# Kernel tuning notes

Measured on AMD Instinct MI355X. Metric: run time of the kernel, lower is better.

## Reference

```python
import jax, jax.numpy as jnp
import numpy as np

P = 1.0  # Yager t-norm exponent (tnorm_p)


def _patches(x, k):
    # x: [B, C, H, W] -> [B, C*k*k, Ho, Wo], feature ordering (c, kh, kw) like torch unfold
    B, C, H, W = x.shape
    Ho, Wo = H - k + 1, W - k + 1
    cols = [x[:, :, i:i + Ho, j:j + Wo] for i in range(k) for j in range(k)]
    p = jnp.stack(cols, axis=2)  # [B, C, k*k, Ho, Wo]
    return p.reshape(B, C * k * k, Ho, Wo)


def _max_yager2d(x, w, p):
    # Fuzzy conv: Yager t-norm T(a,b)=max(0, 1-((1-a)^p+(1-b)^p)^(1/p)) between each
    # patch element and kernel weight, aggregated with max over the receptive field.
    O, C, k, _ = w.shape
    pat = _patches(x, k)                       # [B, L, Ho, Wo], L = C*k*k
    wf = w.reshape(O, -1)                      # [O, L]
    a = 1.0 - pat[:, None]                     # [B, 1, L, Ho, Wo]
    b = 1.0 - wf[None, :, :, None, None]       # [1, O, L, 1, 1]
    t = jnp.maximum(0.0, 1.0 - (a ** p + b ** p) ** (1.0 / p))
    return jnp.max(t, axis=2)                  # [B, O, Ho, Wo]


def _maxpool2(x):
    return jax.lax.reduce_window(x, -jnp.inf, jax.lax.max,
                                 (1, 1, 2, 2), (1, 1, 2, 2), 'VALID')


def setup_inputs() -> dict:
    key = jax.random.key(0)
    k1, k2, k3, k4, k5, k6, k7 = jax.random.split(key, 7)
    B = 128
    inputs = jax.random.uniform(k1, (B, 3, 32, 32), dtype=jnp.float32)
    # fuzzy kernels are membership values in [0,1]
    w1 = jax.random.uniform(k2, (6, 3, 5, 5), dtype=jnp.float32)
    w2 = jax.random.uniform(k3, (16, 6, 5, 5), dtype=jnp.float32)
    w3 = jax.random.uniform(k4, (120, 16, 5, 5), dtype=jnp.float32)
    wd = jax.random.normal(k5, (120, 84), dtype=jnp.float32) * 0.1  # DenseDefuzzy weights
    wf = jax.random.normal(k6, (84, 10), dtype=jnp.float32) * 0.1   # fc5 weight
    bf = jax.random.normal(k7, (10,), dtype=jnp.float32) * 0.01     # fc5 bias
    return {"inputs": inputs, "w1": w1, "w2": w2, "w3": w3,
            "wd": wd, "wf": wf, "bf": bf}


def reference(inputs, w1, w2, w3, wd, wf, bf):
    x = _maxpool2(_max_yager2d(inputs, w1, P))   # [B,6,14,14]
    x = _maxpool2(_max_yager2d(x, w2, P))        # [B,16,5,5]
    x = _max_yager2d(x, w3, P)                   # [B,120,1,1]
    x = x.reshape(x.shape[0], -1)                # [B,120]
    x = jnp.tanh(x @ wd)                         # DenseDefuzzy (unnormalized) + tanh
    return jax.nn.log_softmax(x @ wf + bf, axis=-1)
```

## Files before the change

### kernel.cpp

```cpp
#include <hip/hip_runtime.h>
#include <math.h>


#define NT 1024
#define ROWS 34
#define PLANE (32 * ROWS)

__global__ __launch_bounds__(NT) void fused_lenet(
    const float* __restrict__ x,
    const float* __restrict__ w1,
    const float* __restrict__ w2,
    const float* __restrict__ w3,
    const float* __restrict__ wd,
    const float* __restrict__ wf,
    const float* __restrict__ bfv,
    float* __restrict__ out)
{
    const int img = blockIdx.x;
    const int tid = threadIdx.x;

    __shared__ float s_in[3 * PLANE];
    __shared__ float s_w1d[648];
    __shared__ float s_w2d[3456];
    __shared__ unsigned s_a1u[1176];
    __shared__ unsigned s_a2u[400];
    __shared__ float s_a3[120];
    __shared__ float s_a4[84];

    {
        const float2* src = (const float2*)(x + img * 3072);
        for (int i = tid; i < 1536; i += NT) {
            const int c = i >> 9, rem = i & 511, r = rem >> 4, col2 = rem & 15;
            ((float2*)s_in)[c * (PLANE / 2) + r * (ROWS / 2) + col2] = src[i];
        }
        for (int i = tid; i < 1176; i += NT) s_a1u[i] = 0u;
        if (tid < 400) s_a2u[tid] = 0u;

        for (int e = tid; e < 4104; e += NT) {
            const float* raw;
            float* dst;
            int v;
            if (e < 648) {
                const int oc = e / 108, u = e - oc * 108;
                const int c = u / 36; v = u - c * 36;
                raw = w1 + (oc * 3 + c) * 25;
                dst = s_w1d + e;
            } else {
                const int idx = e - 648;
                const int oc = idx / 216, u = idx - oc * 216;
                const int c = u / 36; v = u - c * 36;
                raw = w2 + (oc * 6 + c) * 25;
                dst = s_w2d + idx;
            }
            const int r = v / 6, col = v - r * 6;
            float m = -1e30f;
            #pragma unroll
            for (int dy = 0; dy < 2; ++dy) {
                const int kh = r - dy;
                if ((unsigned)kh > 4u) continue;
                #pragma unroll
                for (int dx = 0; dx < 2; ++dx) {
                    const int kw = col - dx;
                    if ((unsigned)kw > 4u) continue;
                    m = fmaxf(m, raw[kh * 5 + kw]);
                }
            }
            *dst = m;
        }
    }
    __syncthreads();

    if (tid < 1008) {
        const int c = tid / 336;
        const int rr = tid - c * 336;
        const int oc = rr / 56;
        const int r2 = rr - oc * 56;
        const int py = r2 >> 2;
        const int s = (r2 >> 1) & 1;
        const int h = r2 & 1;
        float acc[7];
        #pragma unroll
        for (int j = 0; j < 7; ++j) acc[j] = -1e30f;
        const float* wbase = s_w1d + (oc * 3 + c) * 36 + h * 18;
        const float* xbase = s_in + c * PLANE + (2 * py + 3 * h) * ROWS + 14 * s;
        #pragma unroll
        for (int u = 0; u < 3; ++u) {
            const float* xr = xbase + u * ROWS;
            float xv[18];
            #pragma unroll
            for (int i2 = 0; i2 < 9; ++i2)
                ((float2*)xv)[i2] = ((const float2*)xr)[i2];
            float wv[6];
            #pragma unroll
            for (int i2 = 0; i2 < 3; ++i2)
                ((float2*)wv)[i2] = ((const float2*)(wbase + u * 6))[i2];
            #pragma unroll
            for (int j = 0; j < 7; ++j) {
                #pragma unroll
                for (int ux = 0; ux < 6; ++ux)
                    acc[j] = fmaxf(acc[j], xv[2 * j + ux] + wv[ux]);
            }
        }
        const int obase = oc * 196 + py * 14 + 7 * s;
        #pragma unroll
        for (int j = 0; j < 7; ++j) {
            const float rl = fmaxf(acc[j] - 1.0f, 0.0f);
            atomicMax(&s_a1u[obase + j], __float_as_uint(rl));
        }
    }
    __syncthreads();

    if (tid < 960) {
        const int oc = tid / 60;
        const int rr = tid - oc * 60;
        const int py = rr / 12;
        const int r2 = rr - py * 12;
        const int c = r2 >> 1;
        const int h = r2 & 1;
        float acc[5];
        #pragma unroll
        for (int j = 0; j < 5; ++j) acc[j] = -1e30f;
        const float* a1f = (const float*)s_a1u;
        const float* wbase = s_w2d + (oc * 6 + c) * 36 + h * 18;
        const float* xbase = a1f + c * 196 + (2 * py + 3 * h) * 14;
        #pragma unroll
        for (int u = 0; u < 3; ++u) {
            const float* xr = xbase + u * 14;
            float xv[14];
            #pragma unroll
            for (int i2 = 0; i2 < 7; ++i2)
                ((float2*)xv)[i2] = ((const float2*)xr)[i2];
            float wv[6];
            #pragma unroll
            for (int i2 = 0; i2 < 3; ++i2)
                ((float2*)wv)[i2] = ((const float2*)(wbase + u * 6))[i2];
            #pragma unroll
            for (int j = 0; j < 5; ++j) {
                #pragma unroll
                for (int ux = 0; ux < 6; ++ux)
                    acc[j] = fmaxf(acc[j], xv[2 * j + ux] + wv[ux]);
            }
        }
        const int obase = oc * 25 + py * 5;
        #pragma unroll
        for (int j = 0; j < 5; ++j) {
            const float rl = fmaxf(acc[j] - 1.0f, 0.0f);
            atomicMax(&s_a2u[obase + j], __float_as_uint(rl));
        }
    }
    __syncthreads();

    if (tid < 960) {
        const int o = tid >> 3, q = tid & 7;
        const float4* wv = (const float4*)(w3 + o * 400);
        const float4* av = (const float4*)(const float*)s_a2u;
        float m = -1e30f;
        for (int l = q; l < 100; l += 8) {
            const float4 w = wv[l];
            const float4 a = av[l];
            m = fmaxf(m, fmaxf(fmaxf(a.x + w.x, a.y + w.y),
                               fmaxf(a.z + w.z, a.w + w.w)));
        }
        m = fmaxf(m, __shfl_xor(m, 1));
        m = fmaxf(m, __shfl_xor(m, 2));
        m = fmaxf(m, __shfl_xor(m, 4));
        if (q == 0) s_a3[o] = fmaxf(m - 1.0f, 0.0f);
    }
    __syncthreads();

    if (tid < 672) {
        const int o = tid >> 3, q = tid & 7;
        float acc = 0.0f;
        #pragma unroll 5
        for (int i = 0; i < 15; ++i) {
            const int k = q * 15 + i;
            acc = fmaf(s_a3[k], wd[k * 84 + o], acc);
        }
        acc += __shfl_xor(acc, 1);
        acc += __shfl_xor(acc, 2);
        acc += __shfl_xor(acc, 4);
        if (q == 0) s_a4[o] = tanhf(acc);
    }
    __syncthreads();

    if (tid < 64) {
        float acc = 0.0f;
        if (tid < 40) {
            const int o = tid >> 2, q = tid & 3;
            #pragma unroll 7
            for (int i = 0; i < 21; ++i) {
                const int k = q * 21 + i;
                acc = fmaf(s_a4[k], wf[k * 10 + o], acc);
            }
            acc += __shfl_xor(acc, 1);
            acc += __shfl_xor(acc, 2);
            acc += bfv[o];
        }
        const float lg = __shfl(acc, (tid < 10) ? tid * 4 : 0);
        if (tid < 16) {
            float v = (tid < 10) ? lg : -1e30f;
            #pragma unroll
            for (int d = 1; d < 16; d <<= 1)
                v = fmaxf(v, __shfl_xor(v, d));
            float e = (tid < 10) ? expf(lg - v) : 0.0f;
            float ssum = e;
            #pragma unroll
            for (int d = 1; d < 16; d <<= 1)
                ssum += __shfl_xor(ssum, d);
            if (tid < 10)
                out[img * 10 + tid] = lg - v - logf(ssum);
        }
    }
}

extern "C" void kernel_launch(void* const* d_in, const int* in_sizes, int n_in,
                              void* d_out, int out_size, void* d_ws, size_t ws_size,
                              hipStream_t stream) {
    const float* x   = (const float*)d_in[0];
    const float* w1  = (const float*)d_in[1];
    const float* w2  = (const float*)d_in[2];
    const float* w3  = (const float*)d_in[3];
    const float* wd  = (const float*)d_in[4];
    const float* wf  = (const float*)d_in[5];
    const float* bfv = (const float*)d_in[6];
    float* out = (float*)d_out;

    const int B = in_sizes[0] / (3 * 32 * 32);
    fused_lenet<<<dim3(B), dim3(NT), 0, stream>>>(
        x, w1, w2, w3, wd, wf, bfv, out);
}
```

Before: 81.91 us.

## Prefetch w3 and wd into registers early and defer w2 preprocessing

Loads the layer-3 weights (13 float4 per thread) into registers at kernel start and the dense weights before the layer-3 barrier, so their global-memory latency overlaps the conv stages instead of stalling the later small stages. Moves the dilated/pooled w2 table build after conv1, so it runs alongside conv1 atomics before the barrier. For the layer-3 loop, out-of-range indices are clamped to the last element, which leaves the max unchanged. The cost is more register pressure (52+15 extra VGPRs) in a 1024-thread block, which risks spills or lower occupancy.

Measured after the change: 78.10 us. 4.6% less time.

```diff
diff --git a/kernel.cpp b/kernel.cpp
--- a/kernel.cpp
+++ b/kernel.cpp
@@ -27,6 +27,17 @@
     __shared__ float s_a3[120];
     __shared__ float s_a4[84];
 
+    float4 w3p[13];
+    if (tid < 960) {
+        const int o = tid >> 3, q = tid & 7;
+        const float4* wv = (const float4*)(w3 + o * 400);
+        #pragma unroll
+        for (int i = 0; i < 13; ++i) {
+            int l = q + 8 * i; if (l > 99) l = 99;
+            w3p[i] = wv[l];
+        }
+    }
+
     {
         const float2* src = (const float2*)(x + img * 3072);
         for (int i = tid; i < 1536; i += NT) {
@@ -35,24 +46,11 @@
         }
         for (int i = tid; i < 1176; i += NT) s_a1u[i] = 0u;
         if (tid < 400) s_a2u[tid] = 0u;
-
-        for (int e = tid; e < 4104; e += NT) {
-            const float* raw;
-            float* dst;
-            int v;
-            if (e < 648) {
-                const int oc = e / 108, u = e - oc * 108;
-                const int c = u / 36; v = u - c * 36;
-                raw = w1 + (oc * 3 + c) * 25;
-                dst = s_w1d + e;
-            } else {
-                const int idx = e - 648;
-                const int oc = idx / 216, u = idx - oc * 216;
-                const int c = u / 36; v = u - c * 36;
-                raw = w2 + (oc * 6 + c) * 25;
-                dst = s_w2d + idx;
-            }
+        if (tid < 648) {
+            const int oc = tid / 108, u = tid - oc * 108;
+            const int c = u / 36, v = u - c * 36;
             const int r = v / 6, col = v - r * 6;
+            const float* raw = w1 + (oc * 3 + c) * 25;
             float m = -1e30f;
             #pragma unroll
             for (int dy = 0; dy < 2; ++dy) {
@@ -65,7 +63,7 @@
                     m = fmaxf(m, raw[kh * 5 + kw]);
                 }
             }
-            *dst = m;
+            s_w1d[tid] = m;
         }
     }
     __syncthreads();
@@ -108,6 +106,25 @@
             atomicMax(&s_a1u[obase + j], __float_as_uint(rl));
         }
     }
+    for (int e = tid; e < 3456; e += NT) {
+        const int oc = e / 216, u = e - oc * 216;
+        const int c = u / 36, v = u - c * 36;
+        const int r = v / 6, col = v - r * 6;
+        const float* raw = w2 + (oc * 6 + c) * 25;
+        float m = -1e30f;
+        #pragma unroll
+        for (int dy = 0; dy < 2; ++dy) {
+            const int kh = r - dy;
+            if ((unsigned)kh > 4u) continue;
+            #pragma unroll
+            for (int dx = 0; dx < 2; ++dx) {
+                const int kw = col - dx;
+                if ((unsigned)kw > 4u) continue;
+                m = fmaxf(m, raw[kh * 5 + kw]);
+            }
+        }
+        s_w2d[e] = m;
+    }
     __syncthreads();
 
     if (tid < 960) {
@@ -148,16 +165,24 @@
             atomicMax(&s_a2u[obase + j], __float_as_uint(rl));
         }
     }
+    float wdp[15];
+    if (tid < 672) {
+        const int o = tid >> 3, q = tid & 7;
+        #pragma unroll
+        for (int i = 0; i < 15; ++i)
+            wdp[i] = wd[(q * 15 + i) * 84 + o];
+    }
     __syncthreads();
 
     if (tid < 960) {
         const int o = tid >> 3, q = tid & 7;
-        const float4* wv = (const float4*)(w3 + o * 400);
         const float4* av = (const float4*)(const float*)s_a2u;
         float m = -1e30f;
-        for (int l = q; l < 100; l += 8) {
-            const float4 w = wv[l];
+        #pragma unroll
+        for (int i = 0; i < 13; ++i) {
+            int l = q + 8 * i; if (l > 99) l = 99;
             const float4 a = av[l];
+            const float4 w = w3p[i];
             m = fmaxf(m, fmaxf(fmaxf(a.x + w.x, a.y + w.y),
                                fmaxf(a.z + w.z, a.w + w.w)));
         }
@@ -171,11 +196,9 @@
     if (tid < 672) {
         const int o = tid >> 3, q = tid & 7;
         float acc = 0.0f;
-        #pragma unroll 5
-        for (int i = 0; i < 15; ++i) {
-            const int k = q * 15 + i;
-            acc = fmaf(s_a3[k], wd[k * 84 + o], acc);
-        }
+        #pragma unroll
+        for (int i = 0; i < 15; ++i)
+            acc = fmaf(s_a3[q * 15 + i], wdp[i], acc);
         acc += __shfl_xor(acc, 1);
         acc += __shfl_xor(acc, 2);
         acc += __shfl_xor(acc, 4);
```
